# Kernel tuning notes

Hardware: AMD Instinct MI355X
Metric: run time of the kernel (lower is better)

The kernel has to match this reference:

```python
import jax, jax.numpy as jnp
import numpy as np

B, S, H = 4, 8192, 512
NH, HD = 8, 64
FD = HD // 2  # random feature dim


def setup_inputs() -> dict:
    key = jax.random.key(0)
    k1, k2, k3, k4 = jax.random.split(key, 4)
    x = jax.random.normal(k1, (B, S, H), dtype=jnp.float32)
    W_qkv = jax.random.normal(k2, (H, 3 * H), dtype=jnp.float32) * (1.0 / np.sqrt(H))
    random_matrix = jax.random.normal(k3, (HD, FD), dtype=jnp.float32) * (1.0 / np.sqrt(HD))
    W_out = jax.random.normal(k4, (H, H), dtype=jnp.float32) * (1.0 / np.sqrt(H))
    b_out = jnp.zeros((H,), dtype=jnp.float32)
    return {"x": x, "W_qkv": W_qkv, "random_matrix": random_matrix,
            "W_out": W_out, "b_out": b_out}


def reference(x, W_qkv, random_matrix, W_out, b_out):
    b, s, h = x.shape
    qkv = (x @ W_qkv).reshape(b, s, 3, NH, HD)
    q, k, v = qkv[:, :, 0], qkv[:, :, 1], qkv[:, :, 2]  # [b,s,nh,hd]
    # Performer-style positive feature map: elu(x @ R) + 1
    q_prime = jax.nn.elu(q @ random_matrix) + 1.0  # [b,s,nh,fd]
    k_prime = jax.nn.elu(k @ random_matrix) + 1.0  # [b,s,nh,fd]
    kv = jnp.einsum('bshd,bshf->bhdf', k_prime, v)          # [b,nh,fd,hd]
    z = jnp.einsum('bshd,bhdf->bshf', q_prime, kv)          # [b,s,nh,hd]
    normalizer = jnp.einsum('bshd,bhd->bsh', q_prime, k_prime.sum(axis=1))
    z = z / (normalizer[..., None] + 1e-6)
    z = z.reshape(b, s, h)
    return z @ W_out + b_out  # dropout is identity in eval
```

## Files before the change

### kernel.cpp

```cpp
#include <hip/hip_runtime.h>


#define DEVFN static __device__ __forceinline__

typedef short short4v __attribute__((ext_vector_type(4)));
typedef short short8 __attribute__((ext_vector_type(8)));
typedef __bf16 bf16x8 __attribute__((ext_vector_type(8)));
typedef float f32x4 __attribute__((ext_vector_type(4)));

DEVFN unsigned short f2bf(float x) {
  unsigned u = __float_as_uint(x);
  u += 0x7FFFu + ((u >> 16) & 1u);
  return (unsigned short)(u >> 16);
}
DEVFN float bf2f(unsigned short s) { return __uint_as_float(((unsigned)s) << 16); }

DEVFN f32x4 mfma16(short8 a, short8 b, f32x4 c) {
  return __builtin_amdgcn_mfma_f32_16x16x32_bf16(
      __builtin_bit_cast(bf16x8, a), __builtin_bit_cast(bf16x8, b), c, 0, 0, 0);
}

DEVFN void gload16(const void* g, void* l) {
  __builtin_amdgcn_global_load_lds((__attribute__((address_space(1))) unsigned*)g,
                                   (__attribute__((address_space(3))) unsigned*)l,
                                   16, 0, 0);
}

__global__ __launch_bounds__(256) void prep(const float* __restrict__ x,
                                            const float* __restrict__ Wqkv,
                                            const float* __restrict__ rm,
                                            unsigned short* __restrict__ xb,
                                            unsigned short* __restrict__ WcatT) {
  const int t = threadIdx.x;
  if (blockIdx.x < 8192) {
    size_t i = ((size_t)blockIdx.x * 256 + t) * 8;
    f32x4 a = *(const f32x4*)(x + i);
    f32x4 b = *(const f32x4*)(x + i + 4);
    short8 o;
    o[0] = (short)f2bf(a[0]); o[1] = (short)f2bf(a[1]);
    o[2] = (short)f2bf(a[2]); o[3] = (short)f2bf(a[3]);
    o[4] = (short)f2bf(b[0]); o[5] = (short)f2bf(b[1]);
    o[6] = (short)f2bf(b[2]); o[7] = (short)f2bf(b[3]);
    *(short8*)(xb + i) = o;
  } else {
    const int n = blockIdx.x - 8192;
    const int h = n >> 7, j = n & 127;
    if (j < 64) {
      const int d = j & 31;
      const int colbase = (j >= 32 ? 512 : 0) + h * 64;
      for (int k = t; k < 512; k += 256) {
        float s = 0.f;
        const float* wrow = Wqkv + (size_t)k * 1536 + colbase;
        #pragma unroll 8
        for (int e = 0; e < 64; ++e) s += wrow[e] * rm[e * 32 + d];
        WcatT[(size_t)n * 512 + k] = f2bf(s);
      }
    } else {
      const int f = j - 64;
      for (int k = t; k < 512; k += 256)
        WcatT[(size_t)n * 512 + k] = f2bf(Wqkv[(size_t)k * 1536 + 1024 + h * 64 + f]);
    }
  }
}

__global__ __launch_bounds__(256) void gemm_qkv(
    const unsigned short* __restrict__ A,
    const unsigned short* __restrict__ BT,
    unsigned short* __restrict__ OQ,
    float* __restrict__ part) {
  __shared__ __attribute__((aligned(16))) unsigned short lds[16384];
  const int t = threadIdx.x;
  const int lane = t & 63, w = t >> 6;
  const int wr = w >> 1, wc = w & 1;
  const int col = lane & 15, kg = lane >> 4;

  const int l = blockIdx.x;
  const int xcd = l & 7, j = l >> 3;
  const int chunk = xcd * 32 + (j >> 3);
  const int h = j & 7;
  const int bh = (chunk >> 6) * 8 + h;

  const long m0 = (long)chunk * 128;
  const unsigned short* ga = A + (m0 + (t >> 2)) * 512 + (t & 3) * 8;
  const unsigned short* gb = BT + ((size_t)h * 128 + (t >> 2)) * 512 + (t & 3) * 8;

  f32x4 acc[4][4] = {};

#define STAGE(buf, kt)                                    \
  {                                                       \
    const int ko_ = (kt) * 32;                            \
    unsigned short* la_ = lds + (buf) * 4096 + w * 512;   \
    unsigned short* lb_ = lds + 8192 + (buf) * 4096 + w * 512; \
    gload16(ga + ko_, la_);                               \
    gload16(ga + 32768 + ko_, la_ + 2048);                \
    gload16(gb + ko_, lb_);                               \
    gload16(gb + 32768 + ko_, lb_ + 2048);                \
  }
  STAGE(0, 0);
  __syncthreads();
  int buf = 0;
  for (int kt = 0; kt < 16; ++kt) {
    if (kt + 1 < 16) STAGE(buf ^ 1, kt + 1);
    const unsigned short* As_ = lds + buf * 4096;
    const unsigned short* Bs_ = lds + 8192 + buf * 4096;
    short8 af[4], bfr[4];
    #pragma unroll
    for (int mi = 0; mi < 4; ++mi)
      af[mi] = *(const short8*)&As_[(wr * 64 + mi * 16 + col) * 32 + kg * 8];
    #pragma unroll
    for (int ni = 0; ni < 4; ++ni)
      bfr[ni] = *(const short8*)&Bs_[(wc * 64 + ni * 16 + col) * 32 + kg * 8];
    #pragma unroll
    for (int mi = 0; mi < 4; ++mi)
      #pragma unroll
      for (int ni = 0; ni < 4; ++ni)
        acc[mi][ni] = mfma16(af[mi], bfr[ni], acc[mi][ni]);
    __syncthreads();
    buf ^= 1;
  }
#undef STAGE

  unsigned short* kT = lds;
  unsigned short* vT = lds + 4480;

  if (wc == 0) {
    #pragma unroll
    for (int ni = 0; ni < 2; ++ni) {
      const int c = h * 32 + ni * 16 + col;
      #pragma unroll
      for (int mi = 0; mi < 4; ++mi)
        #pragma unroll
        for (int r = 0; r < 4; ++r) {
          const long row = m0 + wr * 64 + mi * 16 + kg * 4 + r;
          float v = acc[mi][ni][r];
          v = v > 0.f ? v + 1.f : __expf(v);
          OQ[(size_t)row * 256 + c] = f2bf(v);
        }
    }
    #pragma unroll
    for (int ni = 0; ni < 2; ++ni) {
      const int d = ni * 16 + col;
      #pragma unroll
      for (int mi = 0; mi < 4; ++mi) {
        const int tt0 = wr * 64 + mi * 16 + kg * 4;
        short4v pk;
        #pragma unroll
        for (int r = 0; r < 4; ++r) {
          float v = acc[mi][2 + ni][r];
          v = v > 0.f ? v + 1.f : __expf(v);
          pk[r] = (short)f2bf(v);
        }
        *(short4v*)&kT[d * 140 + tt0] = pk;
      }
    }
  } else {
    #pragma unroll
    for (int ni = 0; ni < 4; ++ni) {
      const int f = ni * 16 + col;
      #pragma unroll
      for (int mi = 0; mi < 4; ++mi) {
        const int tt0 = wr * 64 + mi * 16 + kg * 4;
        short4v pk;
        #pragma unroll
        for (int r = 0; r < 4; ++r) pk[r] = (short)f2bf(acc[mi][ni][r]);
        *(short4v*)&vT[f * 140 + tt0] = pk;
      }
    }
  }
  __syncthreads();

  f32x4 acc_kv[2] = {};
  f32x4 acc_ks[2] = {};
  short8 ones;
  #pragma unroll
  for (int i = 0; i < 8; ++i) ones[i] = (short)0x3F80;
  #pragma unroll
  for (int ks = 0; ks < 4; ++ks) {
    short8 bv = *(const short8*)&vT[(w * 16 + col) * 140 + ks * 32 + kg * 8];
    short8 a0 = *(const short8*)&kT[col * 140 + ks * 32 + kg * 8];
    short8 a1 = *(const short8*)&kT[(16 + col) * 140 + ks * 32 + kg * 8];
    acc_kv[0] = mfma16(a0, bv, acc_kv[0]);
    acc_kv[1] = mfma16(a1, bv, acc_kv[1]);
    if (w == 0) {
      acc_ks[0] = mfma16(a0, ones, acc_ks[0]);
      acc_ks[1] = mfma16(a1, ones, acc_ks[1]);
    }
  }

  float* p = part + ((size_t)bh * 64 + (chunk & 63)) * 2080;
  #pragma unroll
  for (int df = 0; df < 2; ++df)
    #pragma unroll
    for (int r = 0; r < 4; ++r) {
      const int d = df * 16 + kg * 4 + r;
      p[d * 64 + w * 16 + col] = acc_kv[df][r];
    }
  if (w == 0 && col == 0) {
    #pragma unroll
    for (int df = 0; df < 2; ++df)
      #pragma unroll
      for (int r = 0; r < 4; ++r)
        p[2048 + df * 16 + kg * 4 + r] = acc_ks[df][r];
  }
}

__global__ __launch_bounds__(256) void kv_reduce(const float* __restrict__ part,
                                                 float* __restrict__ kvr) {
  const int bh = blockIdx.x, t = threadIdx.x;
  const int idx = blockIdx.y * 256 + t;
  if (idx >= 2080) return;
  float s = 0.f;
  #pragma unroll 8
  for (int c = 0; c < 64; ++c) s += part[((size_t)bh * 64 + c) * 2080 + idx];
  kvr[(size_t)bh * 2080 + idx] = s;
}

__global__ __launch_bounds__(256) void mprep_qn(const float* __restrict__ kvr,
                                                const float* __restrict__ Wout,
                                                const unsigned short* __restrict__ QF,
                                                unsigned short* __restrict__ MT,
                                                unsigned short* __restrict__ QN) {
  const int t = threadIdx.x;
  if (blockIdx.x < 512) {
    __shared__ float Wt[64][33];
    __shared__ float kvt[32][64];
    const int bx = blockIdx.x;
    const int b = bx >> 7, rem = bx & 127;
    const int h = rem >> 4, n0 = (rem & 15) * 32;
    {
      const int f0 = t >> 5, c = t & 31;
      #pragma unroll
      for (int i = 0; i < 8; ++i)
        Wt[f0 + i * 8][c] = Wout[(size_t)(h * 64 + f0 + i * 8) * 512 + n0 + c];
      const float* kvp = kvr + (size_t)(b * 8 + h) * 2080;
      #pragma unroll
      for (int i = 0; i < 2; ++i) {
        const int off = t * 4 + i * 1024;
        f32x4 kk = *(const f32x4*)(kvp + off);
        *(f32x4*)&kvt[off >> 6][off & 63] = kk;
      }
    }
    __syncthreads();
    const int n = t & 31, dg = (t >> 5) * 4;
    float s0 = 0.f, s1 = 0.f, s2 = 0.f, s3 = 0.f;
    #pragma unroll 8
    for (int f = 0; f < 64; ++f) {
      const float wv = Wt[f][n];
      s0 += kvt[dg + 0][f] * wv;
      s1 += kvt[dg + 1][f] * wv;
      s2 += kvt[dg + 2][f] * wv;
      s3 += kvt[dg + 3][f] * wv;
    }
    short4v o;
    o[0] = (short)f2bf(s0); o[1] = (short)f2bf(s1);
    o[2] = (short)f2bf(s2); o[3] = (short)f2bf(s3);
    *(short4v*)&MT[((size_t)b * 512 + n0 + n) * 256 + h * 32 + dg] = o;
  } else {
    __shared__ float ks[256];
    const int bq = blockIdx.x - 512;
    const size_t tid = (size_t)bq * 256 + t;
    const int tok0 = bq * 32;
    const int b = tok0 >> 13;
    ks[t] = kvr[(size_t)(b * 8 + (t >> 5)) * 2080 + 2048 + (t & 31)];
    __syncthreads();
    const int tok = (int)(tid >> 3), h = (int)(tid & 7);
    const short8* q = (const short8*)(QF + (size_t)tok * 256 + h * 32);
    short8 v[4];
    #pragma unroll
    for (int i = 0; i < 4; ++i) v[i] = q[i];
    float den = 1e-6f;
    #pragma unroll
    for (int i = 0; i < 4; ++i)
      #pragma unroll
      for (int j = 0; j < 8; ++j)
        den += bf2f((unsigned short)v[i][j]) * ks[h * 32 + i * 8 + j];
    const float inv = 1.f / den;
    short8* o = (short8*)(QN + (size_t)tok * 256 + h * 32);
    #pragma unroll
    for (int i = 0; i < 4; ++i) {
      short8 ov;
      #pragma unroll
      for (int j = 0; j < 8; ++j)
        ov[j] = (short)f2bf(bf2f((unsigned short)v[i][j]) * inv);
      o[i] = ov;
    }
  }
}

__global__ __launch_bounds__(256) void gemm_out(
    const unsigned short* __restrict__ QN,
    const unsigned short* __restrict__ MT,
    const float* __restrict__ bias,
    float* __restrict__ OC) {
  __shared__ __attribute__((aligned(16))) unsigned short Bls[32768];
  const int t = threadIdx.x;
  const int lane = t & 63, w = t >> 6;
  const int wr = w >> 1, wc = w & 1;
  const int col = lane & 15, kg = lane >> 4;

  const int nx = gridDim.x;
  int wg = blockIdx.y * nx + blockIdx.x;
  const int cpx = (nx * (int)gridDim.y) >> 3;
  wg = (wg & 7) * cpx + (wg >> 3);
  const int bx = wg % nx, by = wg / nx;
  const long m0 = (long)by * 128;
  const long n0 = (long)bx * 128;
  const long b = m0 >> 13;
  const unsigned short* MTb = MT + b * 512 * 256;

  #pragma unroll
  for (int i = 0; i < 16; ++i) {
    const int u = i * 256 + t;
    const int slab = u >> 9, row = (u >> 2) & 127, ch = u & 3;
    gload16(MTb + ((size_t)(n0 + row)) * 256 + slab * 32 + ch * 8,
            Bls + ((size_t)i * 256 + w * 64) * 8);
  }
  __syncthreads();

  f32x4 acc[4][4] = {};
  #pragma unroll 2
  for (int kt = 0; kt < 8; ++kt) {
    short8 af[4], bfr[4];
    #pragma unroll
    for (int mi = 0; mi < 4; ++mi)
      af[mi] = *(const short8*)&QN[(m0 + wr * 64 + mi * 16 + col) * 256 +
                                   kt * 32 + kg * 8];
    #pragma unroll
    for (int ni = 0; ni < 4; ++ni)
      bfr[ni] = *(const short8*)&Bls[kt * 4096 +
                                     (wc * 64 + ni * 16 + col) * 32 + kg * 8];
    #pragma unroll
    for (int mi = 0; mi < 4; ++mi)
      #pragma unroll
      for (int ni = 0; ni < 4; ++ni)
        acc[mi][ni] = mfma16(af[mi], bfr[ni], acc[mi][ni]);
  }

  const int rowb = (int)m0 + wr * 64;
  const int colb = (int)n0 + wc * 64;
  #pragma unroll
  for (int ni = 0; ni < 4; ++ni) {
    const int c = colb + ni * 16 + col;
    const float bb = bias[c];
    #pragma unroll
    for (int mi = 0; mi < 4; ++mi) {
      #pragma unroll
      for (int r = 0; r < 4; ++r) {
        const int row = rowb + mi * 16 + kg * 4 + r;
        OC[(size_t)row * 512 + c] = acc[mi][ni][r] + bb;
      }
    }
  }
}

extern "C" void kernel_launch(void* const* d_in, const int* in_sizes, int n_in,
                              void* d_out, int out_size, void* d_ws, size_t ws_size,
                              hipStream_t stream) {
  const float* x    = (const float*)d_in[0];
  const float* Wqkv = (const float*)d_in[1];
  const float* rm   = (const float*)d_in[2];
  const float* Wout = (const float*)d_in[3];
  const float* bout = (const float*)d_in[4];
  float* out = (float*)d_out;

  char* ws = (char*)d_ws;
  unsigned short* xb    = (unsigned short*)(ws);
  unsigned short* QN    = (unsigned short*)(ws);
  unsigned short* MT    = (unsigned short*)(ws + 16777216);
  unsigned short* WcatT = (unsigned short*)(ws + 33554432);
  unsigned short* QF    = (unsigned short*)(ws + 34603008);
  float* part           = (float*)(ws + 51380224);
  float* kvr            = (float*)(ws + 68419584);

  if (ws_size < 68685824u) return;

  prep<<<dim3(9216), dim3(256), 0, stream>>>(x, Wqkv, rm, xb, WcatT);
  gemm_qkv<<<dim3(2048), dim3(256), 0, stream>>>(xb, WcatT, QF, part);
  kv_reduce<<<dim3(32, 9), dim3(256), 0, stream>>>(part, kvr);
  mprep_qn<<<dim3(1536), dim3(256), 0, stream>>>(kvr, Wout, QF, MT, QN);
  gemm_out<<<dim3(4, 256), dim3(256), 0, stream>>>(QN, MT, bout, out);
}
```

Measured before the change: 132.6 us.

## Fuse fp32-to-bf16 conversion of x into the QKV GEMM tile loads

The prep kernel no longer converts all of x to bf16 in a separate pass. gemm_qkv now streams fp32 x tiles into LDS and converts them to bf16 in registers with v_cvt_pk_bf16_f32 just before the MFMAs. This removes a full write and re-read of a bf16 copy of x, plus most of the prep launch. In exchange each block reads twice as many bytes of A, both from global memory (x is re-read once per head) and from LDS. The LDS footprint grows to 48KB, which may lower occupancy.

```diff
diff --git a/kernel.cpp b/kernel.cpp
--- a/kernel.cpp
+++ b/kernel.cpp
@@ -15,6 +15,18 @@
 }
 DEVFN float bf2f(unsigned short s) { return __uint_as_float(((unsigned)s) << 16); }
 
+DEVFN unsigned cvtpk(float lo, float hi) {
+  unsigned r;
+  asm("v_cvt_pk_bf16_f32 %0, %1, %2" : "=v"(r) : "v"(lo), "v"(hi));
+  return r;
+}
+DEVFN short8 cvt8(f32x4 a, f32x4 b) {
+  union { unsigned u[4]; short8 s; } r;
+  r.u[0] = cvtpk(a[0], a[1]); r.u[1] = cvtpk(a[2], a[3]);
+  r.u[2] = cvtpk(b[0], b[1]); r.u[3] = cvtpk(b[2], b[3]);
+  return r.s;
+}
+
 DEVFN f32x4 mfma16(short8 a, short8 b, f32x4 c) {
   return __builtin_amdgcn_mfma_f32_16x16x32_bf16(
       __builtin_bit_cast(bf16x8, a), __builtin_bit_cast(bf16x8, b), c, 0, 0, 0);
@@ -26,49 +38,35 @@
                                    16, 0, 0);
 }
 
-__global__ __launch_bounds__(256) void prep(const float* __restrict__ x,
-                                            const float* __restrict__ Wqkv,
+__global__ __launch_bounds__(256) void prep(const float* __restrict__ Wqkv,
                                             const float* __restrict__ rm,
-                                            unsigned short* __restrict__ xb,
                                             unsigned short* __restrict__ WcatT) {
   const int t = threadIdx.x;
-  if (blockIdx.x < 8192) {
-    size_t i = ((size_t)blockIdx.x * 256 + t) * 8;
-    f32x4 a = *(const f32x4*)(x + i);
-    f32x4 b = *(const f32x4*)(x + i + 4);
-    short8 o;
-    o[0] = (short)f2bf(a[0]); o[1] = (short)f2bf(a[1]);
-    o[2] = (short)f2bf(a[2]); o[3] = (short)f2bf(a[3]);
-    o[4] = (short)f2bf(b[0]); o[5] = (short)f2bf(b[1]);
-    o[6] = (short)f2bf(b[2]); o[7] = (short)f2bf(b[3]);
-    *(short8*)(xb + i) = o;
+  const int n = blockIdx.x;
+  const int h = n >> 7, j = n & 127;
+  if (j < 64) {
+    const int d = j & 31;
+    const int colbase = (j >= 32 ? 512 : 0) + h * 64;
+    for (int k = t; k < 512; k += 256) {
+      float s = 0.f;
+      const float* wrow = Wqkv + (size_t)k * 1536 + colbase;
+      #pragma unroll 8
+      for (int e = 0; e < 64; ++e) s += wrow[e] * rm[e * 32 + d];
+      WcatT[(size_t)n * 512 + k] = f2bf(s);
+    }
   } else {
-    const int n = blockIdx.x - 8192;
-    const int h = n >> 7, j = n & 127;
-    if (j < 64) {
-      const int d = j & 31;
-      const int colbase = (j >= 32 ? 512 : 0) + h * 64;
-      for (int k = t; k < 512; k += 256) {
-        float s = 0.f;
-        const float* wrow = Wqkv + (size_t)k * 1536 + colbase;
-        #pragma unroll 8
-        for (int e = 0; e < 64; ++e) s += wrow[e] * rm[e * 32 + d];
-        WcatT[(size_t)n * 512 + k] = f2bf(s);
-      }
-    } else {
-      const int f = j - 64;
-      for (int k = t; k < 512; k += 256)
-        WcatT[(size_t)n * 512 + k] = f2bf(Wqkv[(size_t)k * 1536 + 1024 + h * 64 + f]);
-    }
+    const int f = j - 64;
+    for (int k = t; k < 512; k += 256)
+      WcatT[(size_t)n * 512 + k] = f2bf(Wqkv[(size_t)k * 1536 + 1024 + h * 64 + f]);
   }
 }
 
 __global__ __launch_bounds__(256) void gemm_qkv(
-    const unsigned short* __restrict__ A,
+    const float* __restrict__ X,
     const unsigned short* __restrict__ BT,
     unsigned short* __restrict__ OQ,
     float* __restrict__ part) {
-  __shared__ __attribute__((aligned(16))) unsigned short lds[16384];
+  __shared__ __attribute__((aligned(16))) unsigned char lds[49152];
   const int t = threadIdx.x;
   const int lane = t & 63, w = t >> 6;
   const int wr = w >> 1, wc = w & 1;
@@ -81,32 +79,38 @@
   const int bh = (chunk >> 6) * 8 + h;
 
   const long m0 = (long)chunk * 128;
-  const unsigned short* ga = A + (m0 + (t >> 2)) * 512 + (t & 3) * 8;
+  const float* gxa = X + (m0 + w * 32 + (lane >> 3)) * 512 + (lane & 7) * 4;
   const unsigned short* gb = BT + ((size_t)h * 128 + (t >> 2)) * 512 + (t & 3) * 8;
 
   f32x4 acc[4][4] = {};
 
-#define STAGE(buf, kt)                                    \
-  {                                                       \
-    const int ko_ = (kt) * 32;                            \
-    unsigned short* la_ = lds + (buf) * 4096 + w * 512;   \
-    unsigned short* lb_ = lds + 8192 + (buf) * 4096 + w * 512; \
-    gload16(ga + ko_, la_);                               \
-    gload16(ga + 32768 + ko_, la_ + 2048);                \
-    gload16(gb + ko_, lb_);                               \
-    gload16(gb + 32768 + ko_, lb_ + 2048);                \
+#define STAGE(buf, kt)                                      \
+  {                                                         \
+    const int ko_ = (kt) * 32;                              \
+    unsigned char* la_ = lds + (buf) * 16384 + w * 4096;    \
+    unsigned char* lb_ = lds + 32768 + (buf) * 8192 + w * 1024; \
+    gload16(gxa + ko_, la_);                                \
+    gload16(gxa + 8 * 512 + ko_, la_ + 1024);               \
+    gload16(gxa + 16 * 512 + ko_, la_ + 2048);              \
+    gload16(gxa + 24 * 512 + ko_, la_ + 3072);              \
+    gload16(gb + ko_, lb_);                                 \
+    gload16(gb + 64 * 512 + ko_, lb_ + 4096);               \
   }
   STAGE(0, 0);
   __syncthreads();
   int buf = 0;
   for (int kt = 0; kt < 16; ++kt) {
     if (kt + 1 < 16) STAGE(buf ^ 1, kt + 1);
-    const unsigned short* As_ = lds + buf * 4096;
-    const unsigned short* Bs_ = lds + 8192 + buf * 4096;
+    const float* Af = (const float*)(lds + buf * 16384);
+    const unsigned short* Bs_ = (const unsigned short*)(lds + 32768 + buf * 8192);
     short8 af[4], bfr[4];
     #pragma unroll
-    for (int mi = 0; mi < 4; ++mi)
-      af[mi] = *(const short8*)&As_[(wr * 64 + mi * 16 + col) * 32 + kg * 8];
+    for (int mi = 0; mi < 4; ++mi) {
+      const int row = wr * 64 + mi * 16 + col;
+      f32x4 x0 = *(const f32x4*)(Af + row * 32 + kg * 8);
+      f32x4 x1 = *(const f32x4*)(Af + row * 32 + kg * 8 + 4);
+      af[mi] = cvt8(x0, x1);
+    }
     #pragma unroll
     for (int ni = 0; ni < 4; ++ni)
       bfr[ni] = *(const short8*)&Bs_[(wc * 64 + ni * 16 + col) * 32 + kg * 8];
@@ -120,8 +124,8 @@
   }
 #undef STAGE
 
-  unsigned short* kT = lds;
-  unsigned short* vT = lds + 4480;
+  unsigned short* kT = (unsigned short*)lds;
+  unsigned short* vT = (unsigned short*)lds + 4480;
 
   if (wc == 0) {
     #pragma unroll
@@ -364,7 +368,6 @@
   float* out = (float*)d_out;
 
   char* ws = (char*)d_ws;
-  unsigned short* xb    = (unsigned short*)(ws);
   unsigned short* QN    = (unsigned short*)(ws);
   unsigned short* MT    = (unsigned short*)(ws + 16777216);
   unsigned short* WcatT = (unsigned short*)(ws + 33554432);
@@ -374,8 +377,8 @@
 
   if (ws_size < 68685824u) return;
 
-  prep<<<dim3(9216), dim3(256), 0, stream>>>(x, Wqkv, rm, xb, WcatT);
-  gemm_qkv<<<dim3(2048), dim3(256), 0, stream>>>(xb, WcatT, QF, part);
+  prep<<<dim3(1024), dim3(256), 0, stream>>>(Wqkv, rm, WcatT);
+  gemm_qkv<<<dim3(2048), dim3(256), 0, stream>>>(x, WcatT, QF, part);
   kv_reduce<<<dim3(32, 9), dim3(256), 0, stream>>>(part, kvr);
   mprep_qn<<<dim3(1536), dim3(256), 0, stream>>>(kvr, Wout, QF, MT, QN);
   gemm_out<<<dim3(4, 256), dim3(256), 0, stream>>>(QN, MT, bout, out);
```

Measured after the change: 133.1 us. No clear change (+0.4%).
